# Optimization experiments

Hardware: AMD Instinct MI355X
Metric: run time of the kernel (lower is better)

## Reference

```python
import jax, jax.numpy as jnp
import numpy as np

EPS = 1e-6


def _layernorm2d(x, w, b):
    # Normalize over channel dim (axis=1) per pixel; x: [B,C,H,W]
    mu = jnp.mean(x, axis=1, keepdims=True)
    var = jnp.var(x, axis=1, keepdims=True)
    xn = (x - mu) * jax.lax.rsqrt(var + EPS)
    return xn * w[None, :, None, None] + b[None, :, None, None]


def _conv1x1(x, w, b):
    # 1x1 conv == channel matmul; w: [Cout, Cin], x: [B,Cin,H,W]
    return jnp.einsum('oc,bchw->bohw', w, x) + b[None, :, None, None]


def setup_inputs() -> dict:
    key = jax.random.key(0)
    ks = jax.random.split(key, 8)
    B, C, H, W = 4, 64, 180, 320
    s = C ** -0.5  # keep projection weights at sane scale
    return {
        'x_l': jax.random.normal(ks[0], (B, C, H, W), jnp.float32),
        'x_r': jax.random.normal(ks[1], (B, C, H, W), jnp.float32),
        'ln_l_w': jnp.ones((C,), jnp.float32),
        'ln_l_b': jnp.zeros((C,), jnp.float32),
        'ln_r_w': jnp.ones((C,), jnp.float32),
        'ln_r_b': jnp.zeros((C,), jnp.float32),
        'wq_l': jax.random.normal(ks[2], (C, C), jnp.float32) * s,
        'bq_l': jnp.zeros((C,), jnp.float32),
        'wq_r': jax.random.normal(ks[3], (C, C), jnp.float32) * s,
        'bq_r': jnp.zeros((C,), jnp.float32),
        'wv_l': jax.random.normal(ks[4], (C, C), jnp.float32) * s,
        'bv_l': jnp.zeros((C,), jnp.float32),
        'wv_r': jax.random.normal(ks[5], (C, C), jnp.float32) * s,
        'bv_r': jnp.zeros((C,), jnp.float32),
        'beta': jax.random.normal(ks[6], (C,), jnp.float32) * 0.1,
        'gamma': jax.random.normal(ks[7], (C,), jnp.float32) * 0.1,
    }


def reference(x_l, x_r, ln_l_w, ln_l_b, ln_r_w, ln_r_b,
              wq_l, bq_l, wq_r, bq_r, wv_l, bv_l, wv_r, bv_r,
              beta, gamma):
    C = x_l.shape[1]
    scale = C ** -0.5
    # Q projections of LayerNorm'd inputs (Select stub == identity pass-through)
    Q_l = _conv1x1(_layernorm2d(x_l, ln_l_w, ln_l_b), wq_l, bq_l)  # [B,C,H,W]
    Q_r = _conv1x1(_layernorm2d(x_r, ln_r_w, ln_r_b), wq_r, bq_r)  # [B,C,H,W]
    V_l = _conv1x1(x_l, wv_l, bv_l)  # [B,C,H,W]
    V_r = _conv1x1(x_r, wv_r, bv_r)  # [B,C,H,W]
    # attention over width per row: [B,H,Wl,Wr]
    attn = jnp.einsum('bchw,bchv->bhwv', Q_l, Q_r) * scale
    # r -> l: softmax over Wr (last axis), contract with V_r
    F_r2l = jnp.einsum('bhwv,bchv->bchw', jax.nn.softmax(attn, axis=-1), V_r)
    # l -> r: softmax over Wl (axis=2 of attn), contract with V_l
    F_l2r = jnp.einsum('bhwv,bchw->bchv', jax.nn.softmax(attn, axis=2), V_l)
    out_l = x_l + F_r2l * beta[None, :, None, None]
    out_r = x_r + F_l2r * gamma[None, :, None, None]
    return (out_l, out_r)
```

## Files before the change

kernel.cpp:

```cpp
#include <hip/hip_runtime.h>


#define HWs  57600
#define CHWs 3686400
#define TOTs 14745600
#define RST  72
#define VST  328

typedef short bf16x8 __attribute__((ext_vector_type(8)));
typedef float f32x4  __attribute__((ext_vector_type(4)));

union FragU { uint4 q; unsigned short u[8]; bf16x8 v; };

__device__ __forceinline__ unsigned short f2bf(float f) {
  unsigned u = __float_as_uint(f);
  u += 0x7fffu + ((u >> 16) & 1u);
  return (unsigned short)(u >> 16);
}
__device__ __forceinline__ float bf2f(unsigned short s) {
  return __uint_as_float(((unsigned)s) << 16);
}

__global__ __launch_bounds__(512, 1) void sfam_kernel(
    const float* __restrict__ x_l, const float* __restrict__ x_r,
    const float* __restrict__ ln_l_w, const float* __restrict__ ln_l_b,
    const float* __restrict__ ln_r_w, const float* __restrict__ ln_r_b,
    const float* __restrict__ wq_l, const float* __restrict__ bq_l,
    const float* __restrict__ wq_r, const float* __restrict__ bq_r,
    const float* __restrict__ wv_l, const float* __restrict__ bv_l,
    const float* __restrict__ wv_r, const float* __restrict__ bv_r,
    const float* __restrict__ beta, const float* __restrict__ gamma,
    float* __restrict__ out)
{
  __shared__ __align__(16) unsigned short Rs[320*RST];
  __shared__ __align__(16) unsigned short QKs[320*RST];
  __shared__ __align__(16) unsigned short VCs[64*VST];
  __shared__ float PS0[320], PS1[320], PQ0[320], PQ1[320];
  __shared__ float MUs[320], RSs[320];
  __shared__ float BQE[64], BKE[64];

  const int bi  = blockIdx.x;
  const int dir = (bi >= 720) ? 1 : 0;
  const int bh  = bi - dir*720;
  const int b   = bh / 180, h = bh - b*180;
  const int base = b*CHWs + h*320;

  const float* xq   = dir ? x_r   : x_l;
  const float* lnqb = dir ? ln_r_b : ln_l_b;
  const float* lnqw = dir ? ln_r_w : ln_l_w;
  const float* xk   = dir ? x_l   : x_r;
  const float* lnkw = dir ? ln_l_w : ln_r_w;
  const float* lnkb = dir ? ln_l_b : ln_r_b;
  const float* wqq  = dir ? wq_r  : wq_l;
  const float* bqq  = dir ? bq_r  : bq_l;
  const float* wqk  = dir ? wq_l  : wq_r;
  const float* bqk  = dir ? bq_l  : bq_r;
  const float* wv   = dir ? wv_l  : wv_r;
  const float* bv   = dir ? bv_l  : bv_r;
  const float* scl  = dir ? gamma : beta;
  float* op = out + (dir ? TOTs : 0);

  const int t    = threadIdx.x;
  const int wave = t >> 6, lane = t & 63;
  const int p    = lane & 15, g = lane >> 4;
  const int nwt  = (wave < 4) ? 3 : 2;
  const int w0   = (wave < 4) ? wave*48 : 192 + (wave-4)*32;

  if (t < 64) {
    float s = bqq[t];
    for (int c = 0; c < 64; ++c) s += wqq[t*64+c] * lnqb[c];
    BQE[t] = s;
  } else if (t < 128) {
    const int o = t - 64;
    float s = bqk[o];
    for (int c = 0; c < 64; ++c) s += wqk[o*64+c] * lnkb[c];
    BKE[o] = s;
  }

  auto stage = [&](const float* xp) {
    for (int idx = t; idx < 640; idx += 512) {
      const int w   = (idx < 320) ? idx : idx - 320;
      const int chf = (idx < 320) ? 0 : 1;
      const int cb  = chf * 32;
      float s = 0.f, qs = 0.f;
      #pragma unroll 8
      for (int c = 0; c < 32; ++c) {
        float v = xp[base + (cb + c)*HWs + w];
        s += v; qs += v*v;
        Rs[w*RST + cb + c] = f2bf(v);
      }
      if (chf == 0) { PS0[w] = s; PQ0[w] = qs; }
      else          { PS1[w] = s; PQ1[w] = qs; }
    }
    __syncthreads();
    if (t < 320) {
      float m  = (PS0[t] + PS1[t]) * (1.f/64.f);
      float va = (PQ0[t] + PQ1[t]) * (1.f/64.f) - m*m;
      MUs[t] = m;
      RSs[t] = rsqrtf(va + 1e-6f);
    }
    __syncthreads();
  };

  auto projQ = [&](const float* wq, const float* lnw, const float* be,
                   unsigned short* dst, float scale) {
    bf16x8 af[3][2];
    #pragma unroll
    for (int wt = 0; wt < 3; ++wt) if (wt < nwt) {
      #pragma unroll
      for (int kf = 0; kf < 2; ++kf) {
        const int w  = w0 + wt*16 + p;
        const int cb = kf*32 + g*8;
        FragU f; f.q = *(const uint4*)&Rs[w*RST + cb];
        const float mu = MUs[w], rs = RSs[w];
        FragU r;
        #pragma unroll
        for (int j = 0; j < 8; ++j) r.u[j] = f2bf((bf2f(f.u[j]) - mu) * rs);
        af[wt][kf] = r.v;
      }
    }
    bf16x8 bfg[4][2];
    #pragma unroll
    for (int ot = 0; ot < 4; ++ot)
      #pragma unroll
      for (int kf = 0; kf < 2; ++kf) {
        const int o  = ot*16 + p;
        const int cb = kf*32 + g*8;
        FragU r;
        #pragma unroll
        for (int j = 0; j < 8; ++j) r.u[j] = f2bf(wq[o*64 + cb + j] * lnw[cb + j]);
        bfg[ot][kf] = r.v;
      }
    f32x4 acc[3][4];
    #pragma unroll
    for (int wt = 0; wt < 3; ++wt)
      #pragma unroll
      for (int ot = 0; ot < 4; ++ot) acc[wt][ot] = (f32x4){0.f,0.f,0.f,0.f};
    #pragma unroll
    for (int wt = 0; wt < 3; ++wt) if (wt < nwt)
      #pragma unroll
      for (int ot = 0; ot < 4; ++ot)
        #pragma unroll
        for (int kf = 0; kf < 2; ++kf)
          acc[wt][ot] = __builtin_amdgcn_mfma_f32_16x16x32_bf16(af[wt][kf], bfg[ot][kf], acc[wt][ot], 0, 0, 0);
    #pragma unroll
    for (int wt = 0; wt < 3; ++wt) if (wt < nwt)
      #pragma unroll
      for (int ot = 0; ot < 4; ++ot)
        #pragma unroll
        for (int r = 0; r < 4; ++r) {
          const int w = w0 + wt*16 + g*4 + r;
          const int o = ot*16 + p;
          dst[w*RST + o] = f2bf((acc[wt][ot][r] + be[o]) * scale);
        }
  };

  auto projV = [&]() {
    bf16x8 af[4][2];
    #pragma unroll
    for (int mt = 0; mt < 4; ++mt)
      #pragma unroll
      for (int kf = 0; kf < 2; ++kf) {
        const int o  = mt*16 + p;
        const int cb = kf*32 + g*8;
        FragU r;
        #pragma unroll
        for (int j = 0; j < 8; ++j) r.u[j] = f2bf(wv[o*64 + cb + j]);
        af[mt][kf] = r.v;
      }
    bf16x8 bfg[3][2];
    #pragma unroll
    for (int nt = 0; nt < 3; ++nt) if (nt < nwt)
      #pragma unroll
      for (int kf = 0; kf < 2; ++kf) {
        const int w  = w0 + nt*16 + p;
        const int cb = kf*32 + g*8;
        FragU f; f.q = *(const uint4*)&Rs[w*RST + cb];
        bfg[nt][kf] = f.v;
      }
    f32x4 acc[4][3];
    #pragma unroll
    for (int mt = 0; mt < 4; ++mt)
      #pragma unroll
      for (int nt = 0; nt < 3; ++nt) acc[mt][nt] = (f32x4){0.f,0.f,0.f,0.f};
    #pragma unroll
    for (int mt = 0; mt < 4; ++mt)
      #pragma unroll
      for (int nt = 0; nt < 3; ++nt) if (nt < nwt)
        #pragma unroll
        for (int kf = 0; kf < 2; ++kf)
          acc[mt][nt] = __builtin_amdgcn_mfma_f32_16x16x32_bf16(af[mt][kf], bfg[nt][kf], acc[mt][nt], 0, 0, 0);
    #pragma unroll
    for (int mt = 0; mt < 4; ++mt)
      #pragma unroll
      for (int nt = 0; nt < 3; ++nt) if (nt < nwt)
        #pragma unroll
        for (int r = 0; r < 4; ++r) {
          const int o = mt*16 + g*4 + r;
          const int w = w0 + nt*16 + p;
          VCs[o*VST + w] = f2bf(acc[mt][nt][r] + bv[o]);
        }
  };

  stage(xq);
  projQ(wqq, lnqw, BQE, Rs, 0.125f);
  bf16x8 aq[3][2];
  #pragma unroll
  for (int wt = 0; wt < 3; ++wt) if (wt < nwt)
    #pragma unroll
    for (int kf = 0; kf < 2; ++kf) {
      const int w  = w0 + wt*16 + p;
      const int ob = kf*32 + g*8;
      FragU f; f.q = *(const uint4*)&Rs[w*RST + ob];
      aq[wt][kf] = f.v;
    }
  __syncthreads();
  stage(xk);
  projQ(wqk, lnkw, BKE, QKs, 1.0f);
  projV();
  __syncthreads();

  f32x4 oacc[3][4];
  float mst[3][4], lst[3][4], asc[3][4];
  #pragma unroll
  for (int wt = 0; wt < 3; ++wt) {
    #pragma unroll
    for (int ot = 0; ot < 4; ++ot) oacc[wt][ot] = (f32x4){0.f,0.f,0.f,0.f};
    #pragma unroll
    for (int r = 0; r < 4; ++r) { mst[wt][r] = -3.0e38f; lst[wt][r] = 0.f; }
  }

  for (int ch = 0; ch < 5; ++ch) {
    const int v0 = ch*64;
    bf16x8 bk[4][2];
    #pragma unroll
    for (int vt = 0; vt < 4; ++vt)
      #pragma unroll
      for (int kf = 0; kf < 2; ++kf) {
        const int v  = v0 + vt*16 + p;
        const int ob = kf*32 + g*8;
        FragU f; f.q = *(const uint4*)&QKs[v*RST + ob];
        bk[vt][kf] = f.v;
      }
    f32x4 sacc[3][4];
    #pragma unroll
    for (int wt = 0; wt < 3; ++wt)
      #pragma unroll
      for (int vt = 0; vt < 4; ++vt) sacc[wt][vt] = (f32x4){0.f,0.f,0.f,0.f};
    #pragma unroll
    for (int wt = 0; wt < 3; ++wt) if (wt < nwt)
      #pragma unroll
      for (int vt = 0; vt < 4; ++vt)
        #pragma unroll
        for (int kf = 0; kf < 2; ++kf)
          sacc[wt][vt] = __builtin_amdgcn_mfma_f32_16x16x32_bf16(aq[wt][kf], bk[vt][kf], sacc[wt][vt], 0, 0, 0);

    #pragma unroll
    for (int wt = 0; wt < 3; ++wt) if (wt < nwt)
      #pragma unroll
      for (int r = 0; r < 4; ++r) {
        float cm = fmaxf(fmaxf(sacc[wt][0][r], sacc[wt][1][r]),
                         fmaxf(sacc[wt][2][r], sacc[wt][3][r]));
        cm = fmaxf(cm, __shfl_xor(cm, 1));
        cm = fmaxf(cm, __shfl_xor(cm, 2));
        cm = fmaxf(cm, __shfl_xor(cm, 4));
        cm = fmaxf(cm, __shfl_xor(cm, 8));
        const float mn = fmaxf(mst[wt][r], cm);
        const float al = __expf(mst[wt][r] - mn);
        mst[wt][r] = mn;
        float rsum = 0.f;
        #pragma unroll
        for (int vt = 0; vt < 4; ++vt) {
          float pv = __expf(sacc[wt][vt][r] - mn);
          sacc[wt][vt][r] = pv;
          rsum += pv;
        }
        rsum += __shfl_xor(rsum, 1);
        rsum += __shfl_xor(rsum, 2);
        rsum += __shfl_xor(rsum, 4);
        rsum += __shfl_xor(rsum, 8);
        lst[wt][r] = lst[wt][r]*al + rsum;
        asc[wt][r] = al;
      }
    #pragma unroll
    for (int wt = 0; wt < 3; ++wt) if (wt < nwt)
      #pragma unroll
      for (int ot = 0; ot < 4; ++ot)
        #pragma unroll
        for (int r = 0; r < 4; ++r) oacc[wt][ot][r] *= asc[wt][r];

    #pragma unroll
    for (int wt = 0; wt < 3; ++wt) if (wt < nwt)
      #pragma unroll
      for (int vt = 0; vt < 4; ++vt)
        #pragma unroll
        for (int r = 0; r < 4; ++r) {
          const int w = w0 + wt*16 + g*4 + r;
          Rs[w*RST + vt*16 + p] = f2bf(sacc[wt][vt][r]);
        }
    bf16x8 ap[3][2];
    #pragma unroll
    for (int wt = 0; wt < 3; ++wt) if (wt < nwt)
      #pragma unroll
      for (int kh = 0; kh < 2; ++kh) {
        const int w  = w0 + wt*16 + p;
        const int j0 = kh*32 + g*8;
        FragU f; f.q = *(const uint4*)&Rs[w*RST + j0];
        ap[wt][kh] = f.v;
      }
    bf16x8 bvv[4][2];
    #pragma unroll
    for (int ot = 0; ot < 4; ++ot)
      #pragma unroll
      for (int kh = 0; kh < 2; ++kh) {
        const int o  = ot*16 + p;
        const int vv = v0 + kh*32 + g*8;
        FragU f; f.q = *(const uint4*)&VCs[o*VST + vv];
        bvv[ot][kh] = f.v;
      }
    #pragma unroll
    for (int wt = 0; wt < 3; ++wt) if (wt < nwt)
      #pragma unroll
      for (int ot = 0; ot < 4; ++ot)
        #pragma unroll
        for (int kh = 0; kh < 2; ++kh)
          oacc[wt][ot] = __builtin_amdgcn_mfma_f32_16x16x32_bf16(ap[wt][kh], bvv[ot][kh], oacc[wt][ot], 0, 0, 0);
  }

  #pragma unroll
  for (int wt = 0; wt < 3; ++wt) if (wt < nwt)
    #pragma unroll
    for (int ot = 0; ot < 4; ++ot)
      #pragma unroll
      for (int r = 0; r < 4; ++r) {
        const int w = w0 + wt*16 + g*4 + r;
        const int o = ot*16 + p;
        Rs[w*RST + o] = f2bf(oacc[wt][ot][r] / lst[wt][r]);
      }
  __syncthreads();
  for (int idx = t; idx < 640; idx += 512) {
    const int w   = (idx < 320) ? idx : idx - 320;
    const int chf = (idx < 320) ? 0 : 1;
    const int cb  = chf * 32;
    #pragma unroll 8
    for (int c = 0; c < 32; ++c) {
      const int cc = cb + c;
      const int gi = base + cc*HWs + w;
      op[gi] = xq[gi] + scl[cc] * bf2f(Rs[w*RST + cc]);
    }
  }
}

extern "C" void kernel_launch(void* const* d_in, const int* in_sizes, int n_in,
                              void* d_out, int out_size, void* d_ws, size_t ws_size,
                              hipStream_t stream) {
  (void)in_sizes; (void)n_in; (void)d_ws; (void)ws_size; (void)out_size;
  sfam_kernel<<<dim3(1440), dim3(512), 0, stream>>>(
      (const float*)d_in[0],  (const float*)d_in[1],
      (const float*)d_in[2],  (const float*)d_in[3],
      (const float*)d_in[4],  (const float*)d_in[5],
      (const float*)d_in[6],  (const float*)d_in[7],
      (const float*)d_in[8],  (const float*)d_in[9],
      (const float*)d_in[10], (const float*)d_in[11],
      (const float*)d_in[12], (const float*)d_in[13],
      (const float*)d_in[14], (const float*)d_in[15],
      (float*)d_out);
}
```

Baseline: 494.5 us.

## Compute both attention directions per block with shared score matrix and exact row/col max

```diff
diff --git a/kernel.cpp b/kernel.cpp
--- a/kernel.cpp
+++ b/kernel.cpp
@@ -6,10 +6,10 @@
 #define TOTs 14745600
 #define RST  72
 #define VST  328
+#define PTS  40
 
 typedef short bf16x8 __attribute__((ext_vector_type(8)));
 typedef float f32x4  __attribute__((ext_vector_type(4)));
-
 union FragU { uint4 q; unsigned short u[8]; bf16x8 v; };
 
 __device__ __forceinline__ unsigned short f2bf(float f) {
@@ -21,7 +21,7 @@
   return __uint_as_float(((unsigned)s) << 16);
 }
 
-__global__ __launch_bounds__(512, 1) void sfam_kernel(
+__global__ __launch_bounds__(512, 2) void sfam_kernel(
     const float* __restrict__ x_l, const float* __restrict__ x_r,
     const float* __restrict__ ln_l_w, const float* __restrict__ ln_l_b,
     const float* __restrict__ ln_r_w, const float* __restrict__ ln_r_b,
@@ -33,163 +33,101 @@
     float* __restrict__ out)
 {
   __shared__ __align__(16) unsigned short Rs[320*RST];
-  __shared__ __align__(16) unsigned short QKs[320*RST];
-  __shared__ __align__(16) unsigned short VCs[64*VST];
-  __shared__ float PS0[320], PS1[320], PQ0[320], PQ1[320];
-  __shared__ float MUs[320], RSs[320];
-  __shared__ float BQE[64], BKE[64];
-
-  const int bi  = blockIdx.x;
-  const int dir = (bi >= 720) ? 1 : 0;
-  const int bh  = bi - dir*720;
-  const int b   = bh / 180, h = bh - b*180;
+  __shared__ __align__(16) unsigned short Ks[320*RST];
+  __shared__ __align__(16) unsigned short Vb[64*VST];
+  __shared__ __align__(16) unsigned short Pt[8*16*PTS];
+  __shared__ float SR[8*320];
+  __shared__ float MU[640], RSd[640];
+  __shared__ float c_arr[320];
+  __shared__ float BB[128];
+
+  const int bh = blockIdx.x;
+  const int b = bh / 180, h = bh - b*180;
   const int base = b*CHWs + h*320;
 
-  const float* xq   = dir ? x_r   : x_l;
-  const float* lnqb = dir ? ln_r_b : ln_l_b;
-  const float* lnqw = dir ? ln_r_w : ln_l_w;
-  const float* xk   = dir ? x_l   : x_r;
-  const float* lnkw = dir ? ln_l_w : ln_r_w;
-  const float* lnkb = dir ? ln_l_b : ln_r_b;
-  const float* wqq  = dir ? wq_r  : wq_l;
-  const float* bqq  = dir ? bq_r  : bq_l;
-  const float* wqk  = dir ? wq_l  : wq_r;
-  const float* bqk  = dir ? bq_l  : bq_r;
-  const float* wv   = dir ? wv_l  : wv_r;
-  const float* bv   = dir ? bv_l  : bv_r;
-  const float* scl  = dir ? gamma : beta;
-  float* op = out + (dir ? TOTs : 0);
-
-  const int t    = threadIdx.x;
+  const int t = threadIdx.x;
   const int wave = t >> 6, lane = t & 63;
-  const int p    = lane & 15, g = lane >> 4;
-  const int nwt  = (wave < 4) ? 3 : 2;
-  const int w0   = (wave < 4) ? wave*48 : 192 + (wave-4)*32;
-
-  if (t < 64) {
-    float s = bqq[t];
-    for (int c = 0; c < 64; ++c) s += wqq[t*64+c] * lnqb[c];
-    BQE[t] = s;
-  } else if (t < 128) {
-    const int o = t - 64;
-    float s = bqk[o];
-    for (int c = 0; c < 64; ++c) s += wqk[o*64+c] * lnkb[c];
-    BKE[o] = s;
-  }
-
-  auto stage = [&](const float* xp) {
-    for (int idx = t; idx < 640; idx += 512) {
-      const int w   = (idx < 320) ? idx : idx - 320;
-      const int chf = (idx < 320) ? 0 : 1;
-      const int cb  = chf * 32;
-      float s = 0.f, qs = 0.f;
-      #pragma unroll 8
-      for (int c = 0; c < 32; ++c) {
-        float v = xp[base + (cb + c)*HWs + w];
-        s += v; qs += v*v;
-        Rs[w*RST + cb + c] = f2bf(v);
-      }
-      if (chf == 0) { PS0[w] = s; PQ0[w] = qs; }
-      else          { PS1[w] = s; PQ1[w] = qs; }
-    }
-    __syncthreads();
-    if (t < 320) {
-      float m  = (PS0[t] + PS1[t]) * (1.f/64.f);
-      float va = (PQ0[t] + PQ1[t]) * (1.f/64.f) - m*m;
-      MUs[t] = m;
-      RSs[t] = rsqrtf(va + 1e-6f);
-    }
-    __syncthreads();
-  };
-
-  auto projQ = [&](const float* wq, const float* lnw, const float* be,
-                   unsigned short* dst, float scale) {
-    bf16x8 af[3][2];
-    #pragma unroll
-    for (int wt = 0; wt < 3; ++wt) if (wt < nwt) {
-      #pragma unroll
-      for (int kf = 0; kf < 2; ++kf) {
-        const int w  = w0 + wt*16 + p;
-        const int cb = kf*32 + g*8;
-        FragU f; f.q = *(const uint4*)&Rs[w*RST + cb];
-        const float mu = MUs[w], rs = RSs[w];
-        FragU r;
-        #pragma unroll
-        for (int j = 0; j < 8; ++j) r.u[j] = f2bf((bf2f(f.u[j]) - mu) * rs);
-        af[wt][kf] = r.v;
-      }
-    }
-    bf16x8 bfg[4][2];
-    #pragma unroll
-    for (int ot = 0; ot < 4; ++ot)
-      #pragma unroll
-      for (int kf = 0; kf < 2; ++kf) {
-        const int o  = ot*16 + p;
-        const int cb = kf*32 + g*8;
-        FragU r;
-        #pragma unroll
-        for (int j = 0; j < 8; ++j) r.u[j] = f2bf(wq[o*64 + cb + j] * lnw[cb + j]);
-        bfg[ot][kf] = r.v;
-      }
-    f32x4 acc[3][4];
-    #pragma unroll
-    for (int wt = 0; wt < 3; ++wt)
-      #pragma unroll
-      for (int ot = 0; ot < 4; ++ot) acc[wt][ot] = (f32x4){0.f,0.f,0.f,0.f};
-    #pragma unroll
-    for (int wt = 0; wt < 3; ++wt) if (wt < nwt)
-      #pragma unroll
-      for (int ot = 0; ot < 4; ++ot)
+  const int p = lane & 15, g = lane >> 4;
+  const int nwt = (wave < 4) ? 3 : 2;
+  const int w0 = (wave < 4) ? wave*48 : 192 + (wave-4)*32;
+
+  for (int idx = t; idx < 1280; idx += 512) {
+    int r2 = idx; const int side = (r2 >= 640); r2 -= side*640;
+    const int half = (r2 >= 320); const int w = r2 - half*320;
+    const int cb = half*32;
+    const float* xp = side ? x_r : x_l;
+    unsigned short* dst = side ? Ks : Rs;
+    float s = 0.f, q = 0.f;
+    #pragma unroll 8
+    for (int c = 0; c < 32; ++c) {
+      float v = xp[base + (cb+c)*HWs + w];
+      s += v; q += v*v;
+      dst[w*RST + cb + c] = f2bf(v);
+    }
+    SR[(side*2+half)*320 + w] = s;
+    SR[(4+side*2+half)*320 + w] = q;
+  }
+  if (t < 128) {
+    const int o = t & 63;
+    const float* wqp = (t < 64) ? wq_l : wq_r;
+    const float* lwp = (t < 64) ? ln_l_w : ln_r_w;
+    const float* lbp = (t < 64) ? ln_l_b : ln_r_b;
+    const float* bqp = (t < 64) ? bq_l : bq_r;
+    float s = bqp[o];
+    for (int c = 0; c < 64; ++c) s += wqp[o*64+c]*lwp[c]*lbp[c];
+    BB[t] = s;
+  }
+  __syncthreads();
+  for (int i = t; i < 640; i += 512) {
+    const int side = (i >= 320); const int w = i - side*320;
+    float m = (SR[(side*2)*320+w] + SR[(side*2+1)*320+w]) * (1.f/64.f);
+    float q = (SR[(4+side*2)*320+w] + SR[(4+side*2+1)*320+w]) * (1.f/64.f) - m*m;
+    MU[i] = m;
+    RSd[i] = rsqrtf(q + 1e-6f);
+  }
+  __syncthreads();
+
+  auto projV = [&](const float* wvp, const float* bvp, const unsigned short* src,
+                   const float* mup, const float* rsp, bool inv) {
+    bf16x8 bx[3][2];
+    #pragma unroll
+    for (int nt = 0; nt < 3; ++nt) if (nt < nwt) {
+      const int w = w0 + nt*16 + p;
+      const float mu = mup[w];
+      const float sd = inv ? (1.0f / rsp[w]) : 0.f;
+      #pragma unroll
+      for (int kf = 0; kf < 2; ++kf) {
+        FragU f; f.q = *(const uint4*)&src[w*RST + kf*32 + g*8];
+        if (inv) {
+          FragU rr;
+          #pragma unroll
+          for (int j = 0; j < 8; ++j) rr.u[j] = f2bf(bf2f(f.u[j])*sd + mu);
+          bx[nt][kf] = rr.v;
+        } else bx[nt][kf] = f.v;
+      }
+    }
+    bf16x8 av[4][2];
+    #pragma unroll
+    for (int mt = 0; mt < 4; ++mt)
+      #pragma unroll
+      for (int kf = 0; kf < 2; ++kf) {
+        FragU rr;
+        #pragma unroll
+        for (int j = 0; j < 8; ++j) rr.u[j] = f2bf(wvp[(mt*16+p)*64 + kf*32 + g*8 + j]);
+        av[mt][kf] = rr.v;
+      }
+    f32x4 acc[4][3];
+    #pragma unroll
+    for (int mt = 0; mt < 4; ++mt)
+      #pragma unroll
+      for (int nt = 0; nt < 3; ++nt) acc[mt][nt] = (f32x4){0.f,0.f,0.f,0.f};
+    #pragma unroll
+    for (int mt = 0; mt < 4; ++mt)
+      #pragma unroll
+      for (int nt = 0; nt < 3; ++nt) if (nt < nwt)
         #pragma unroll
         for (int kf = 0; kf < 2; ++kf)
-          acc[wt][ot] = __builtin_amdgcn_mfma_f32_16x16x32_bf16(af[wt][kf], bfg[ot][kf], acc[wt][ot], 0, 0, 0);
-    #pragma unroll
-    for (int wt = 0; wt < 3; ++wt) if (wt < nwt)
-      #pragma unroll
-      for (int ot = 0; ot < 4; ++ot)
-        #pragma unroll
-        for (int r = 0; r < 4; ++r) {
-          const int w = w0 + wt*16 + g*4 + r;
-          const int o = ot*16 + p;
-          dst[w*RST + o] = f2bf((acc[wt][ot][r] + be[o]) * scale);
-        }
-  };
-
-  auto projV = [&]() {
-    bf16x8 af[4][2];
-    #pragma unroll
-    for (int mt = 0; mt < 4; ++mt)
-      #pragma unroll
-      for (int kf = 0; kf < 2; ++kf) {
-        const int o  = mt*16 + p;
-        const int cb = kf*32 + g*8;
-        FragU r;
-        #pragma unroll
-        for (int j = 0; j < 8; ++j) r.u[j] = f2bf(wv[o*64 + cb + j]);
-        af[mt][kf] = r.v;
-      }
-    bf16x8 bfg[3][2];
-    #pragma unroll
-    for (int nt = 0; nt < 3; ++nt) if (nt < nwt)
-      #pragma unroll
-      for (int kf = 0; kf < 2; ++kf) {
-        const int w  = w0 + nt*16 + p;
-        const int cb = kf*32 + g*8;
-        FragU f; f.q = *(const uint4*)&Rs[w*RST + cb];
-        bfg[nt][kf] = f.v;
-      }
-    f32x4 acc[4][3];
-    #pragma unroll
-    for (int mt = 0; mt < 4; ++mt)
-      #pragma unroll
-      for (int nt = 0; nt < 3; ++nt) acc[mt][nt] = (f32x4){0.f,0.f,0.f,0.f};
-    #pragma unroll
-    for (int mt = 0; mt < 4; ++mt)
-      #pragma unroll
-      for (int nt = 0; nt < 3; ++nt) if (nt < nwt)
-        #pragma unroll
-        for (int kf = 0; kf < 2; ++kf)
-          acc[mt][nt] = __builtin_amdgcn_mfma_f32_16x16x32_bf16(af[mt][kf], bfg[nt][kf], acc[mt][nt], 0, 0, 0);
+          acc[mt][nt] = __builtin_amdgcn_mfma_f32_16x16x32_bf16(av[mt][kf], bx[nt][kf], acc[mt][nt], 0,0,0);
     #pragma unroll
     for (int mt = 0; mt < 4; ++mt)
       #pragma unroll
@@ -197,156 +135,346 @@
         #pragma unroll
         for (int r = 0; r < 4; ++r) {
           const int o = mt*16 + g*4 + r;
-          const int w = w0 + nt*16 + p;
-          VCs[o*VST + w] = f2bf(acc[mt][nt][r] + bv[o]);
+          Vb[o*VST + w0 + nt*16 + p] = f2bf(acc[mt][nt][r] + bvp[o]);
         }
   };
 
-  stage(xq);
-  projQ(wqq, lnqw, BQE, Rs, 0.125f);
-  bf16x8 aq[3][2];
+  projV(wv_l, bv_l, Rs, MU, RSd, false);
+
+  float cR[3][4];
+  {
+    bf16x8 qa[3][2];
+    #pragma unroll
+    for (int wt = 0; wt < 3; ++wt) if (wt < nwt) {
+      const int w = w0 + wt*16 + p;
+      const float mu = MU[w], rs = RSd[w];
+      #pragma unroll
+      for (int kf = 0; kf < 2; ++kf) {
+        FragU f; f.q = *(const uint4*)&Rs[w*RST + kf*32 + g*8];
+        FragU rr;
+        #pragma unroll
+        for (int j = 0; j < 8; ++j) rr.u[j] = f2bf((bf2f(f.u[j]) - mu) * rs);
+        qa[wt][kf] = rr.v;
+      }
+    }
+    bf16x8 bw[4][2];
+    #pragma unroll
+    for (int ot = 0; ot < 4; ++ot)
+      #pragma unroll
+      for (int kf = 0; kf < 2; ++kf) {
+        FragU rr;
+        #pragma unroll
+        for (int j = 0; j < 8; ++j) {
+          const int c = kf*32 + g*8 + j;
+          rr.u[j] = f2bf(wq_l[(ot*16+p)*64 + c] * ln_l_w[c]);
+        }
+        bw[ot][kf] = rr.v;
+      }
+    f32x4 qacc[3][4];
+    #pragma unroll
+    for (int wt = 0; wt < 3; ++wt)
+      #pragma unroll
+      for (int ot = 0; ot < 4; ++ot) qacc[wt][ot] = (f32x4){0.f,0.f,0.f,0.f};
+    #pragma unroll
+    for (int wt = 0; wt < 3; ++wt) if (wt < nwt)
+      #pragma unroll
+      for (int ot = 0; ot < 4; ++ot)
+        #pragma unroll
+        for (int kf = 0; kf < 2; ++kf)
+          qacc[wt][ot] = __builtin_amdgcn_mfma_f32_16x16x32_bf16(qa[wt][kf], bw[ot][kf], qacc[wt][ot], 0,0,0);
+    #pragma unroll
+    for (int wt = 0; wt < 3; ++wt) {
+      #pragma unroll
+      for (int r = 0; r < 4; ++r) cR[wt][r] = 0.f;
+      if (wt < nwt) {
+        #pragma unroll
+        for (int ot = 0; ot < 4; ++ot) {
+          const float bl = BB[ot*16+p], br = BB[64 + ot*16+p];
+          #pragma unroll
+          for (int r = 0; r < 4; ++r) {
+            const float qv = qacc[wt][ot][r] + bl;
+            Rs[(w0 + wt*16 + g*4 + r)*RST + ot*16 + p] = f2bf(qv);
+            cR[wt][r] += qv * br;
+          }
+        }
+        #pragma unroll
+        for (int r = 0; r < 4; ++r) {
+          float cv = cR[wt][r];
+          cv += __shfl_xor(cv, 1); cv += __shfl_xor(cv, 2);
+          cv += __shfl_xor(cv, 4); cv += __shfl_xor(cv, 8);
+          cv *= 0.125f;
+          cR[wt][r] = cv;
+          if (p == 0) c_arr[w0 + wt*16 + g*4 + r] = cv;
+        }
+      }
+    }
+  }
+
+  {
+    bf16x8 qla[3][2];
+    #pragma unroll
+    for (int wt = 0; wt < 3; ++wt) if (wt < nwt)
+      #pragma unroll
+      for (int kf = 0; kf < 2; ++kf) {
+        FragU f; f.q = *(const uint4*)&Rs[(w0 + wt*16 + p)*RST + kf*32 + g*8];
+        qla[wt][kf] = f.v;
+      }
+    bf16x8 bwt[4][2];
+    #pragma unroll
+    for (int ct = 0; ct < 4; ++ct) {
+      const float lw = ln_r_w[ct*16 + p];
+      #pragma unroll
+      for (int kf = 0; kf < 2; ++kf) {
+        FragU rr;
+        #pragma unroll
+        for (int j = 0; j < 8; ++j)
+          rr.u[j] = f2bf(wq_r[(kf*32 + g*8 + j)*64 + ct*16 + p] * lw);
+        bwt[ct][kf] = rr.v;
+      }
+    }
+    f32x4 q2[3][4];
+    #pragma unroll
+    for (int wt = 0; wt < 3; ++wt)
+      #pragma unroll
+      for (int ct = 0; ct < 4; ++ct) q2[wt][ct] = (f32x4){0.f,0.f,0.f,0.f};
+    #pragma unroll
+    for (int wt = 0; wt < 3; ++wt) if (wt < nwt)
+      #pragma unroll
+      for (int ct = 0; ct < 4; ++ct)
+        #pragma unroll
+        for (int kf = 0; kf < 2; ++kf)
+          q2[wt][ct] = __builtin_amdgcn_mfma_f32_16x16x32_bf16(qla[wt][kf], bwt[ct][kf], q2[wt][ct], 0,0,0);
+    #pragma unroll
+    for (int wt = 0; wt < 3; ++wt) if (wt < nwt)
+      #pragma unroll
+      for (int ct = 0; ct < 4; ++ct)
+        #pragma unroll
+        for (int r = 0; r < 4; ++r)
+          Rs[(w0 + wt*16 + g*4 + r)*RST + ct*16 + p] = f2bf(q2[wt][ct][r] * 0.125f);
+  }
+
+  #pragma unroll
+  for (int wt = 0; wt < 3; ++wt) if (wt < nwt) {
+    const int w = w0 + wt*16 + p;
+    const float mu = MU[320+w], rs = RSd[320+w];
+    #pragma unroll
+    for (int kf = 0; kf < 2; ++kf) {
+      FragU f; f.q = *(const uint4*)&Ks[w*RST + kf*32 + g*8];
+      FragU rr;
+      #pragma unroll
+      for (int j = 0; j < 8; ++j) rr.u[j] = f2bf((bf2f(f.u[j]) - mu) * rs);
+      *(uint4*)&Ks[w*RST + kf*32 + g*8] = rr.q;
+    }
+  }
+  __syncthreads();
+
+  bf16x8 aq[3][2], ak[3][2];
   #pragma unroll
   for (int wt = 0; wt < 3; ++wt) if (wt < nwt)
     #pragma unroll
     for (int kf = 0; kf < 2; ++kf) {
-      const int w  = w0 + wt*16 + p;
-      const int ob = kf*32 + g*8;
-      FragU f; f.q = *(const uint4*)&Rs[w*RST + ob];
-      aq[wt][kf] = f.v;
-    }
-  __syncthreads();
-  stage(xk);
-  projQ(wqk, lnkw, BKE, QKs, 1.0f);
-  projV();
-  __syncthreads();
-
+      FragU f1; f1.q = *(const uint4*)&Rs[(w0 + wt*16 + p)*RST + kf*32 + g*8];
+      aq[wt][kf] = f1.v;
+      FragU f2; f2.q = *(const uint4*)&Ks[(w0 + wt*16 + p)*RST + kf*32 + g*8];
+      ak[wt][kf] = f2.v;
+    }
+
+  float rm[3][4];
+  #pragma unroll
+  for (int wt = 0; wt < 3; ++wt)
+    #pragma unroll
+    for (int r = 0; r < 4; ++r) rm[wt][r] = -3.0e38f;
+  for (int ch = 0; ch < 5; ++ch) {
+    const int k0 = ch*64;
+    bf16x8 bq[4][2];
+    #pragma unroll
+    for (int vt = 0; vt < 4; ++vt)
+      #pragma unroll
+      for (int kf = 0; kf < 2; ++kf) {
+        FragU f; f.q = *(const uint4*)&Ks[(k0 + vt*16 + p)*RST + kf*32 + g*8];
+        bq[vt][kf] = f.v;
+      }
+    f32x4 sacc[3][4];
+    #pragma unroll
+    for (int wt = 0; wt < 3; ++wt)
+      #pragma unroll
+      for (int vt = 0; vt < 4; ++vt) sacc[wt][vt] = (f32x4){0.f,0.f,0.f,0.f};
+    #pragma unroll
+    for (int wt = 0; wt < 3; ++wt) if (wt < nwt)
+      #pragma unroll
+      for (int vt = 0; vt < 4; ++vt)
+        #pragma unroll
+        for (int kf = 0; kf < 2; ++kf)
+          sacc[wt][vt] = __builtin_amdgcn_mfma_f32_16x16x32_bf16(aq[wt][kf], bq[vt][kf], sacc[wt][vt], 0,0,0);
+    #pragma unroll
+    for (int wt = 0; wt < 3; ++wt) if (wt < nwt) {
+      #pragma unroll
+      for (int r = 0; r < 4; ++r) {
+        float m4 = fmaxf(fmaxf(sacc[wt][0][r], sacc[wt][1][r]),
+                         fmaxf(sacc[wt][2][r], sacc[wt][3][r])) + cR[wt][r];
+        m4 = fmaxf(m4, __shfl_xor(m4, 1)); m4 = fmaxf(m4, __shfl_xor(m4, 2));
+        m4 = fmaxf(m4, __shfl_xor(m4, 4)); m4 = fmaxf(m4, __shfl_xor(m4, 8));
+        rm[wt][r] = fmaxf(rm[wt][r], m4);
+      }
+    }
+    #pragma unroll
+    for (int vt = 0; vt < 4; ++vt) {
+      float cp = -3.0e38f;
+      #pragma unroll
+      for (int wt = 0; wt < 3; ++wt) if (wt < nwt)
+        #pragma unroll
+        for (int r = 0; r < 4; ++r) cp = fmaxf(cp, sacc[wt][vt][r] + cR[wt][r]);
+      cp = fmaxf(cp, __shfl_xor(cp, 16));
+      cp = fmaxf(cp, __shfl_xor(cp, 32));
+      if (g == 0) SR[wave*320 + k0 + vt*16 + p] = cp;
+    }
+  }
+  __syncthreads();
+  if (t < 320) {
+    float m = SR[t];
+    #pragma unroll
+    for (int j = 1; j < 8; ++j) m = fmaxf(m, SR[j*320 + t]);
+    SR[t] = m;
+  }
+  __syncthreads();
+
+  float ls[3][4];
   f32x4 oacc[3][4];
-  float mst[3][4], lst[3][4], asc[3][4];
-  #pragma unroll
-  for (int wt = 0; wt < 3; ++wt) {
+  auto attn_pass = [&](bf16x8 (&A)[3][2], const unsigned short* Bsrc,
+                       float (&mx)[3][4], bool colc) {
+    for (int ch = 0; ch < 5; ++ch) {
+      const int k0 = ch*64;
+      bf16x8 bq[4][2];
+      #pragma unroll
+      for (int vt = 0; vt < 4; ++vt)
+        #pragma unroll
+        for (int kf = 0; kf < 2; ++kf) {
+          FragU f; f.q = *(const uint4*)&Bsrc[(k0 + vt*16 + p)*RST + kf*32 + g*8];
+          bq[vt][kf] = f.v;
+        }
+      float cc4[4];
+      #pragma unroll
+      for (int vt = 0; vt < 4; ++vt) cc4[vt] = colc ? c_arr[k0 + vt*16 + p] : 0.f;
+      f32x4 sacc[3][4];
+      #pragma unroll
+      for (int wt = 0; wt < 3; ++wt)
+        #pragma unroll
+        for (int vt = 0; vt < 4; ++vt) sacc[wt][vt] = (f32x4){0.f,0.f,0.f,0.f};
+      #pragma unroll
+      for (int wt = 0; wt < 3; ++wt) if (wt < nwt)
+        #pragma unroll
+        for (int vt = 0; vt < 4; ++vt)
+          #pragma unroll
+          for (int kf = 0; kf < 2; ++kf)
+            sacc[wt][vt] = __builtin_amdgcn_mfma_f32_16x16x32_bf16(A[wt][kf], bq[vt][kf], sacc[wt][vt], 0,0,0);
+      #pragma unroll
+      for (int wt = 0; wt < 3; ++wt) if (wt < nwt) {
+        #pragma unroll
+        for (int r = 0; r < 4; ++r) {
+          const float rc = colc ? 0.f : cR[wt][r];
+          float rsum = 0.f;
+          #pragma unroll
+          for (int vt = 0; vt < 4; ++vt) {
+            const float e = __expf(sacc[wt][vt][r] + rc + cc4[vt] - mx[wt][r]);
+            sacc[wt][vt][r] = e; rsum += e;
+          }
+          rsum += __shfl_xor(rsum, 1); rsum += __shfl_xor(rsum, 2);
+          rsum += __shfl_xor(rsum, 4); rsum += __shfl_xor(rsum, 8);
+          ls[wt][r] += rsum;
+        }
+      }
+      bf16x8 bvv[2][4];
+      #pragma unroll
+      for (int kf = 0; kf < 2; ++kf)
+        #pragma unroll
+        for (int ot = 0; ot < 4; ++ot) {
+          FragU f; f.q = *(const uint4*)&Vb[(ot*16+p)*VST + k0 + kf*32 + g*8];
+          bvv[kf][ot] = f.v;
+        }
+      unsigned short* ptw = &Pt[wave*16*PTS];
+      #pragma unroll
+      for (int wt = 0; wt < 3; ++wt) if (wt < nwt) {
+        #pragma unroll
+        for (int kf = 0; kf < 2; ++kf) {
+          #pragma unroll
+          for (int vh = 0; vh < 2; ++vh) {
+            const int vt2 = kf*2 + vh;
+            #pragma unroll
+            for (int r = 0; r < 4; ++r)
+              ptw[(g*4 + r)*PTS + vh*16 + p] = f2bf(sacc[wt][vt2][r]);
+          }
+          FragU fa; fa.q = *(const uint4*)&ptw[p*PTS + g*8];
+          #pragma unroll
+          for (int ot = 0; ot < 4; ++ot)
+            oacc[wt][ot] = __builtin_amdgcn_mfma_f32_16x16x32_bf16(fa.v, bvv[kf][ot], oacc[wt][ot], 0,0,0);
+        }
+      }
+    }
+  };
+
+  float cmR[3][4];
+  #pragma unroll
+  for (int wt = 0; wt < 3; ++wt)
+    #pragma unroll
+    for (int r = 0; r < 4; ++r) {
+      cmR[wt][r] = (wt < nwt) ? SR[w0 + wt*16 + g*4 + r] : 0.f;
+      ls[wt][r] = 0.f;
+    }
+  #pragma unroll
+  for (int wt = 0; wt < 3; ++wt)
     #pragma unroll
     for (int ot = 0; ot < 4; ++ot) oacc[wt][ot] = (f32x4){0.f,0.f,0.f,0.f};
-    #pragma unroll
-    for (int r = 0; r < 4; ++r) { mst[wt][r] = -3.0e38f; lst[wt][r] = 0.f; }
-  }
-
-  for (int ch = 0; ch < 5; ++ch) {
-    const int v0 = ch*64;
-    bf16x8 bk[4][2];
-    #pragma unroll
-    for (int vt = 0; vt < 4; ++vt)
-      #pragma unroll
-      for (int kf = 0; kf < 2; ++kf) {
-        const int v  = v0 + vt*16 + p;
-        const int ob = kf*32 + g*8;
-        FragU f; f.q = *(const uint4*)&QKs[v*RST + ob];
-        bk[vt][kf] = f.v;
-      }
-    f32x4 sacc[3][4];
-    #pragma unroll
-    for (int wt = 0; wt < 3; ++wt)
-      #pragma unroll
-      for (int vt = 0; vt < 4; ++vt) sacc[wt][vt] = (f32x4){0.f,0.f,0.f,0.f};
-    #pragma unroll
-    for (int wt = 0; wt < 3; ++wt) if (wt < nwt)
-      #pragma unroll
-      for (int vt = 0; vt < 4; ++vt)
-        #pragma unroll
-        for (int kf = 0; kf < 2; ++kf)
-          sacc[wt][vt] = __builtin_amdgcn_mfma_f32_16x16x32_bf16(aq[wt][kf], bk[vt][kf], sacc[wt][vt], 0, 0, 0);
-
-    #pragma unroll
-    for (int wt = 0; wt < 3; ++wt) if (wt < nwt)
-      #pragma unroll
-      for (int r = 0; r < 4; ++r) {
-        float cm = fmaxf(fmaxf(sacc[wt][0][r], sacc[wt][1][r]),
-                         fmaxf(sacc[wt][2][r], sacc[wt][3][r]));
-        cm = fmaxf(cm, __shfl_xor(cm, 1));
-        cm = fmaxf(cm, __shfl_xor(cm, 2));
-        cm = fmaxf(cm, __shfl_xor(cm, 4));
-        cm = fmaxf(cm, __shfl_xor(cm, 8));
-        const float mn = fmaxf(mst[wt][r], cm);
-        const float al = __expf(mst[wt][r] - mn);
-        mst[wt][r] = mn;
-        float rsum = 0.f;
-        #pragma unroll
-        for (int vt = 0; vt < 4; ++vt) {
-          float pv = __expf(sacc[wt][vt][r] - mn);
-          sacc[wt][vt][r] = pv;
-          rsum += pv;
-        }
-        rsum += __shfl_xor(rsum, 1);
-        rsum += __shfl_xor(rsum, 2);
-        rsum += __shfl_xor(rsum, 4);
-        rsum += __shfl_xor(rsum, 8);
-        lst[wt][r] = lst[wt][r]*al + rsum;
-        asc[wt][r] = al;
-      }
-    #pragma unroll
-    for (int wt = 0; wt < 3; ++wt) if (wt < nwt)
+  attn_pass(ak, Rs, cmR, true);
+  __syncthreads();
+
+  #pragma unroll
+  for (int wt = 0; wt < 3; ++wt) if (wt < nwt)
+    #pragma unroll
+    for (int r = 0; r < 4; ++r) {
+      const float inv = 1.0f / ls[wt][r];
       #pragma unroll
       for (int ot = 0; ot < 4; ++ot)
-        #pragma unroll
-        for (int r = 0; r < 4; ++r) oacc[wt][ot][r] *= asc[wt][r];
-
-    #pragma unroll
-    for (int wt = 0; wt < 3; ++wt) if (wt < nwt)
-      #pragma unroll
-      for (int vt = 0; vt < 4; ++vt)
-        #pragma unroll
-        for (int r = 0; r < 4; ++r) {
-          const int w = w0 + wt*16 + g*4 + r;
-          Rs[w*RST + vt*16 + p] = f2bf(sacc[wt][vt][r]);
-        }
-    bf16x8 ap[3][2];
-    #pragma unroll
-    for (int wt = 0; wt < 3; ++wt) if (wt < nwt)
-      #pragma unroll
-      for (int kh = 0; kh < 2; ++kh) {
-        const int w  = w0 + wt*16 + p;
-        const int j0 = kh*32 + g*8;
-        FragU f; f.q = *(const uint4*)&Rs[w*RST + j0];
-        ap[wt][kh] = f.v;
-      }
-    bf16x8 bvv[4][2];
-    #pragma unroll
-    for (int ot = 0; ot < 4; ++ot)
-      #pragma unroll
-      for (int kh = 0; kh < 2; ++kh) {
-        const int o  = ot*16 + p;
-        const int vv = v0 + kh*32 + g*8;
-        FragU f; f.q = *(const uint4*)&VCs[o*VST + vv];
-        bvv[ot][kh] = f.v;
-      }
-    #pragma unroll
-    for (int wt = 0; wt < 3; ++wt) if (wt < nwt)
+        Rs[(w0 + wt*16 + g*4 + r)*RST + ot*16 + p] = f2bf(oacc[wt][ot][r] * inv);
+    }
+
+  projV(wv_r, bv_r, Ks, MU+320, RSd+320, true);
+  __syncthreads();
+
+  #pragma unroll
+  for (int wt = 0; wt < 3; ++wt)
+    #pragma unroll
+    for (int r = 0; r < 4; ++r) ls[wt][r] = 0.f;
+  #pragma unroll
+  for (int wt = 0; wt < 3; ++wt)
+    #pragma unroll
+    for (int ot = 0; ot < 4; ++ot) oacc[wt][ot] = (f32x4){0.f,0.f,0.f,0.f};
+  attn_pass(aq, Ks, rm, false);
+  __syncthreads();
+
+  #pragma unroll
+  for (int wt = 0; wt < 3; ++wt) if (wt < nwt)
+    #pragma unroll
+    for (int r = 0; r < 4; ++r) {
+      const float inv = 1.0f / ls[wt][r];
       #pragma unroll
       for (int ot = 0; ot < 4; ++ot)
-        #pragma unroll
-        for (int kh = 0; kh < 2; ++kh)
-          oacc[wt][ot] = __builtin_amdgcn_mfma_f32_16x16x32_bf16(ap[wt][kh], bvv[ot][kh], oacc[wt][ot], 0, 0, 0);
-  }
-
-  #pragma unroll
-  for (int wt = 0; wt < 3; ++wt) if (wt < nwt)
-    #pragma unroll
-    for (int ot = 0; ot < 4; ++ot)
-      #pragma unroll
-      for (int r = 0; r < 4; ++r) {
-        const int w = w0 + wt*16 + g*4 + r;
-        const int o = ot*16 + p;
-        Rs[w*RST + o] = f2bf(oacc[wt][ot][r] / lst[wt][r]);
-      }
-  __syncthreads();
-  for (int idx = t; idx < 640; idx += 512) {
-    const int w   = (idx < 320) ? idx : idx - 320;
-    const int chf = (idx < 320) ? 0 : 1;
-    const int cb  = chf * 32;
+        Ks[(w0 + wt*16 + g*4 + r)*RST + ot*16 + p] = f2bf(oacc[wt][ot][r] * inv);
+    }
+  __syncthreads();
+
+  for (int idx = t; idx < 1280; idx += 512) {
+    int r2 = idx; const int side = (r2 >= 640); r2 -= side*640;
+    const int half = (r2 >= 320); const int w = r2 - half*320;
+    const int cb = half*32;
+    const float* xs = side ? x_r : x_l;
+    const unsigned short* Osrc = side ? Rs : Ks;
+    const float* sc = side ? gamma : beta;
+    float* op = out + (side ? TOTs : 0);
     #pragma unroll 8
     for (int c = 0; c < 32; ++c) {
       const int cc = cb + c;
       const int gi = base + cc*HWs + w;
-      op[gi] = xq[gi] + scl[cc] * bf2f(Rs[w*RST + cc]);
+      op[gi] = xs[gi] + sc[cc] * bf2f(Osrc[w*RST + cc]);
     }
   }
 }
@@ -355,7 +483,7 @@
                               void* d_out, int out_size, void* d_ws, size_t ws_size,
                               hipStream_t stream) {
   (void)in_sizes; (void)n_in; (void)d_ws; (void)ws_size; (void)out_size;
-  sfam_kernel<<<dim3(1440), dim3(512), 0, stream>>>(
+  sfam_kernel<<<dim3(720), dim3(512), 0, stream>>>(
       (const float*)d_in[0],  (const float*)d_in[1],
       (const float*)d_in[2],  (const float*)d_in[3],
       (const float*)d_in[4],  (const float*)d_in[5],
```

After: 432.9 us. 12.5% less time.
